# Kernel tuning notes

Measured on AMD Instinct MI355X. Metric: run time of the kernel, lower is better.

Reference implementation:

```python
import jax, jax.numpy as jnp
import numpy as np

N, K, M, D = 50000, 32, 50000, 128  # dst nodes, neighbors, src nodes, hidden_dim


def setup_inputs() -> dict:
    key = jax.random.key(0)
    k1, k2, k3, k4 = jax.random.split(key, 4)
    nei = jax.random.randint(k1, (N, K), 0, M, dtype=jnp.int64)
    h = jax.random.normal(k2, (M, D), dtype=jnp.float32)
    h_refer = jax.random.normal(k3, (N, D), dtype=jnp.float32)
    # xavier_normal_ on (1, 2D) with gain=1.414: std = gain*sqrt(2/(1+2D))
    std = 1.414 * np.sqrt(2.0 / (1 + 2 * D))
    att = jax.random.normal(k4, (1, 2 * D), dtype=jnp.float32) * std
    return {"nei": nei, "h": h, "h_refer": h_refer, "att": att}


def reference(nei, h, h_refer, att):
    # gather neighbor embeddings: [N, K, D]
    nei_emb = h[nei]
    # split att so we never materialize the concatenated [N, K, 2D] tensor:
    # cat([h_refer, nei_emb], -1) @ att.T == h_refer @ att_ref + nei_emb @ att_nei
    att_ref = att[0, :D]   # [D]
    att_nei = att[0, D:]   # [D]
    scores = (h_refer @ att_ref)[:, None] + jnp.einsum("nkd,d->nk", nei_emb, att_nei)  # [N, K]
    scores = jax.nn.leaky_relu(scores, negative_slope=0.01)
    w = jax.nn.softmax(scores, axis=1)  # softmax over neighbors
    # weighted sum over neighbors -> [N, D]
    return jnp.einsum("nk,nkd->nd", w, nei_emb)
```

## Files before the change

kernel.cpp:

```cpp
#include <hip/hip_runtime.h>

typedef unsigned int uint32;
typedef unsigned long long uint64;
typedef unsigned short ushort_t;
typedef _Float16 h2_t __attribute__((ext_vector_type(2)));
typedef float f32x2 __attribute__((ext_vector_type(2)));

#define KNEI 32
#define DIM 128
#define WPB 4

enum { SRC_BF16 = 0, SRC_F16 = 1, SRC_F32 = 2 };

__device__ __forceinline__ float bflo(uint32 u) {
    union { uint32 u; float f; } c; c.u = u << 16; return c.f;
}
__device__ __forceinline__ float bfhi(uint32 u) {
    union { uint32 u; float f; } c; c.u = u & 0xffff0000u; return c.f;
}
__device__ __forceinline__ uint32 pack_bf16_rne(float a, float b) {
    union { float f; uint32 u; } x, y; x.f = a; y.f = b;
    uint32 ua = (x.u + 0x7fffu + ((x.u >> 16) & 1u)) >> 16;
    uint32 ub = (y.u + 0x7fffu + ((y.u >> 16) & 1u)) >> 16;
    return (ua & 0xffffu) | (ub << 16);
}
__device__ __forceinline__ uint32 pack_f16(float a, float b) {
    union { h2_t h; uint32 u; } c;
    c.h.x = (_Float16)a; c.h.y = (_Float16)b;
    return c.u;
}
__device__ __forceinline__ h2_t as_h2(uint32 u) {
    union { uint32 u; h2_t h; } c; c.u = u; return c.h;
}

__device__ __forceinline__ bool probe_bf16(const void* h, int lane) {
    const uint32 hs = ((const uint32*)h)[lane];
    const uint32 e  = (hs >> 7) & 0xFFu;
    const bool  tb  = (e >= 90u) && (e <= 140u);
    return (__ballot(tb) == ~0ull);
}

template<int SRC>
__device__ __forceinline__ void run_row(
    const void* __restrict__ hsv, const void* __restrict__ hrv,
    const void* __restrict__ attv, void* __restrict__ outv,
    const void* __restrict__ neiv, bool i64, int Mrows, int n, int lane)
{
    constexpr bool F32 = (SRC != SRC_BF16);
    const int r4 = lane >> 4;
    const int c  = lane & 15;

    int idxv;
    if (i64) idxv = (int)__builtin_nontemporal_load(
                        (const long long*)neiv + (size_t)n * KNEI + (lane & 31));
    else     idxv = __builtin_nontemporal_load(
                        (const int*)neiv + (size_t)n * KNEI + (lane & 31));
    idxv = min(max(idxv, 0), Mrows - 1);

    int rows[8];
    #pragma unroll
    for (int it = 0; it < 8; ++it)
        rows[it] = __shfl(idxv, it * 4 + r4, 64);

    uint4 ev[8];
    #pragma unroll
    for (int it = 0; it < 8; ++it) {
        if constexpr (SRC == SRC_F32) {
            const float4* sp = (const float4*)hsv + ((size_t)rows[it] << 5) + c * 2;
            const float4 p0 = sp[0], p1 = sp[1];
            ev[it].x = pack_f16(p0.x, p0.y);
            ev[it].y = pack_f16(p0.z, p0.w);
            ev[it].z = pack_f16(p1.x, p1.y);
            ev[it].w = pack_f16(p1.z, p1.w);
        } else {
            ev[it] = *((const uint4*)hsv + ((size_t)rows[it] << 4) + c);
        }
    }

    float base;
    {
        float b0, b1, a0, a1;
        if (F32) {
            const f32x2 hp = __builtin_nontemporal_load(
                (const f32x2*)((const float*)hrv + (size_t)n * DIM) + lane);
            const float2 ap = *((const float2*)attv + lane);
            b0 = hp.x; b1 = hp.y; a0 = ap.x; a1 = ap.y;
        } else {
            const uint32 hu = __builtin_nontemporal_load(
                (const uint32*)((const ushort_t*)hrv + (size_t)n * DIM) + lane);
            const uint32 au = ((const uint32*)attv)[lane];
            b0 = bflo(hu); b1 = bfhi(hu); a0 = bflo(au); a1 = bfhi(au);
        }
        base = b0 * a0 + b1 * a1;
        #pragma unroll
        for (int off = 32; off >= 1; off >>= 1)
            base += __shfl_xor(base, off, 64);
    }

    float an[8];
    if (F32) {
        const float4* ap = (const float4*)((const float*)attv + DIM + c * 8);
        const float4 p0 = ap[0], p1 = ap[1];
        an[0] = p0.x; an[1] = p0.y; an[2] = p0.z; an[3] = p0.w;
        an[4] = p1.x; an[5] = p1.y; an[6] = p1.z; an[7] = p1.w;
    } else {
        const uint4 au = *((const uint4*)((const ushort_t*)attv + DIM) + c);
        an[0] = bflo(au.x); an[1] = bfhi(au.x); an[2] = bflo(au.y); an[3] = bfhi(au.y);
        an[4] = bflo(au.z); an[5] = bfhi(au.z); an[6] = bflo(au.w); an[7] = bfhi(au.w);
    }

    float s[8];
    #pragma unroll
    for (int it = 0; it < 8; ++it) {
        const uint4 e = ev[it];
        if constexpr (SRC == SRC_BF16) {
            s[it] = bflo(e.x) * an[0] + bfhi(e.x) * an[1]
                  + bflo(e.y) * an[2] + bfhi(e.y) * an[3]
                  + bflo(e.z) * an[4] + bfhi(e.z) * an[5]
                  + bflo(e.w) * an[6] + bfhi(e.w) * an[7];
        } else {
            const h2_t e0 = as_h2(e.x), e1 = as_h2(e.y), e2 = as_h2(e.z), e3 = as_h2(e.w);
            const float t0 = fmaf((float)e0.x, an[0],
                             fmaf((float)e0.y, an[1],
                             fmaf((float)e1.x, an[2], (float)e1.y * an[3])));
            const float t1 = fmaf((float)e2.x, an[4],
                             fmaf((float)e2.y, an[5],
                             fmaf((float)e3.x, an[6], (float)e3.y * an[7])));
            s[it] = t0 + t1;
        }
    }
    #pragma unroll
    for (int off = 1; off <= 8; off <<= 1) {
        #pragma unroll
        for (int it = 0; it < 8; ++it)
            s[it] += __shfl_xor(s[it], off, 64);
    }
    #pragma unroll
    for (int it = 0; it < 8; ++it) {
        const float v = base + s[it];
        s[it] = (v > 0.f) ? v : 0.01f * v;
    }

    float m = s[0];
    #pragma unroll
    for (int it = 1; it < 8; ++it) m = fmaxf(m, s[it]);
    m = fmaxf(m, __shfl_xor(m, 16, 64));
    m = fmaxf(m, __shfl_xor(m, 32, 64));

    float w[8];
    float sum = 0.f;
    #pragma unroll
    for (int it = 0; it < 8; ++it) { w[it] = __expf(s[it] - m); sum += w[it]; }
    sum += __shfl_xor(sum, 16, 64);
    sum += __shfl_xor(sum, 32, 64);
    const float inv = 1.0f / sum;

    float acc[8] = {0.f, 0.f, 0.f, 0.f, 0.f, 0.f, 0.f, 0.f};
    #pragma unroll
    for (int it = 0; it < 8; ++it) {
        const float wk = w[it] * inv;
        const uint4 e = ev[it];
        if constexpr (SRC == SRC_BF16) {
            acc[0] = fmaf(wk, bflo(e.x), acc[0]);
            acc[1] = fmaf(wk, bfhi(e.x), acc[1]);
            acc[2] = fmaf(wk, bflo(e.y), acc[2]);
            acc[3] = fmaf(wk, bfhi(e.y), acc[3]);
            acc[4] = fmaf(wk, bflo(e.z), acc[4]);
            acc[5] = fmaf(wk, bfhi(e.z), acc[5]);
            acc[6] = fmaf(wk, bflo(e.w), acc[6]);
            acc[7] = fmaf(wk, bfhi(e.w), acc[7]);
        } else {
            const h2_t e0 = as_h2(e.x), e1 = as_h2(e.y), e2 = as_h2(e.z), e3 = as_h2(e.w);
            acc[0] = fmaf(wk, (float)e0.x, acc[0]);
            acc[1] = fmaf(wk, (float)e0.y, acc[1]);
            acc[2] = fmaf(wk, (float)e1.x, acc[2]);
            acc[3] = fmaf(wk, (float)e1.y, acc[3]);
            acc[4] = fmaf(wk, (float)e2.x, acc[4]);
            acc[5] = fmaf(wk, (float)e2.y, acc[5]);
            acc[6] = fmaf(wk, (float)e3.x, acc[6]);
            acc[7] = fmaf(wk, (float)e3.y, acc[7]);
        }
    }
    #pragma unroll
    for (int d = 0; d < 8; ++d) acc[d] += __shfl_xor(acc[d], 16, 64);
    #pragma unroll
    for (int d = 0; d < 8; ++d) acc[d] += __shfl_xor(acc[d], 32, 64);

    const float q0a = (r4 & 2) ? acc[4] : acc[0];
    const float q0b = (r4 & 2) ? acc[5] : acc[1];
    const float q1a = (r4 & 2) ? acc[6] : acc[2];
    const float q1b = (r4 & 2) ? acc[7] : acc[3];
    const float o0 = (r4 & 1) ? q1a : q0a;
    const float o1 = (r4 & 1) ? q1b : q0b;

    if (F32) {
        f32x2 o; o.x = o0; o.y = o1;
        *((f32x2*)((float*)outv + (size_t)n * DIM) + c * 4 + r4) = o;
    } else {
        ((uint32*)((ushort_t*)outv + (size_t)n * DIM))[c * 4 + r4] = pack_bf16_rne(o0, o1);
    }
}

__global__ __launch_bounds__(256) void gat_kernel(
    const void* __restrict__ nei, const void* __restrict__ h,
    const void* __restrict__ h_refer, const void* __restrict__ att,
    void* __restrict__ out, const void* __restrict__ hf16,
    int N, int Mrows, int use_ws)
{
    const int tid  = threadIdx.x;
    const int lane = tid & 63;
    const int n    = blockIdx.x * WPB + (tid >> 6);

    const bool is_bf16 = probe_bf16(h, lane);
    const uint32 nhi = ((const uint32*)nei)[2 * lane + 1];
    const bool  i64  = (__ballot(nhi == 0u) == ~0ull);

    if (n >= N) return;

    if (is_bf16)     run_row<SRC_BF16>(h,    h_refer, att, out, nei, i64, Mrows, n, lane);
    else if (use_ws) run_row<SRC_F16 >(hf16, h_refer, att, out, nei, i64, Mrows, n, lane);
    else             run_row<SRC_F32 >(h,    h_refer, att, out, nei, i64, Mrows, n, lane);
}

__global__ __launch_bounds__(256) void conv_kernel(
    const void* __restrict__ h, uint4* __restrict__ ws, long long ngroups)
{
    if (probe_bf16(h, threadIdx.x & 63)) return;
    const long long i = (long long)blockIdx.x * 256 + threadIdx.x;
    if (i >= ngroups) return;
    const float4* sp = (const float4*)h + i * 2;
    const float4 p0 = sp[0], p1 = sp[1];
    uint4 o;
    o.x = pack_f16(p0.x, p0.y);
    o.y = pack_f16(p0.z, p0.w);
    o.z = pack_f16(p1.x, p1.y);
    o.w = pack_f16(p1.z, p1.w);
    ws[i] = o;
}

extern "C" void kernel_launch(void* const* d_in, const int* in_sizes, int n_in,
                              void* d_out, int out_size, void* d_ws, size_t ws_size,
                              hipStream_t stream) {
    const int N = out_size / DIM;
    const int M = in_sizes[1] / DIM;

    const size_t need = (size_t)M * DIM * sizeof(ushort_t);
    const int use_ws = (d_ws != nullptr && ws_size >= need) ? 1 : 0;

    if (use_ws) {
        const long long ngroups = (long long)M * (DIM / 8);
        dim3 cg((unsigned)((ngroups + 255) / 256)), cb(256);
        conv_kernel<<<cg, cb, 0, stream>>>(d_in[1], (uint4*)d_ws, ngroups);
    }

    dim3 grid((N + WPB - 1) / WPB), block(64 * WPB);
    gat_kernel<<<grid, block, 0, stream>>>(d_in[0], d_in[1], d_in[2], d_in[3],
                                           d_out, d_ws, N, M, use_ws);
}
```

Measured before the change: 150.5 us.

## Process two destination rows per wavefront to double gathers in flight

Each wavefront now handles two destination nodes. It loads all 64 neighbor indices in one load and issues the gathers for both rows before computing either, which doubles memory-level parallelism per wave. The h_refer dot product for both rows is computed together, and stores and conv loads become nontemporal. In exchange, register pressure rises because 16 uint4 gather buffers are live at once, which may reduce occupancy, and the grid has half as many waves.

```diff
diff --git a/kernel.cpp b/kernel.cpp
--- a/kernel.cpp
+++ b/kernel.cpp
@@ -4,11 +4,14 @@
 typedef unsigned long long uint64;
 typedef unsigned short ushort_t;
 typedef _Float16 h2_t __attribute__((ext_vector_type(2)));
-typedef float f32x2 __attribute__((ext_vector_type(2)));
+typedef float  f32x2 __attribute__((ext_vector_type(2)));
+typedef float  f32x4 __attribute__((ext_vector_type(4)));
+typedef uint32 u32x2 __attribute__((ext_vector_type(2)));
 
 #define KNEI 32
 #define DIM 128
 #define WPB 4
+#define RPW 2
 
 enum { SRC_BF16 = 0, SRC_F16 = 1, SRC_F32 = 2 };
 
@@ -41,73 +44,11 @@
 }
 
 template<int SRC>
-__device__ __forceinline__ void run_row(
-    const void* __restrict__ hsv, const void* __restrict__ hrv,
-    const void* __restrict__ attv, void* __restrict__ outv,
-    const void* __restrict__ neiv, bool i64, int Mrows, int n, int lane)
+__device__ __forceinline__ void process_row(
+    const uint4* ev, const float* an, float base,
+    void* __restrict__ outv, size_t n, int lane, int r4, int c)
 {
     constexpr bool F32 = (SRC != SRC_BF16);
-    const int r4 = lane >> 4;
-    const int c  = lane & 15;
-
-    int idxv;
-    if (i64) idxv = (int)__builtin_nontemporal_load(
-                        (const long long*)neiv + (size_t)n * KNEI + (lane & 31));
-    else     idxv = __builtin_nontemporal_load(
-                        (const int*)neiv + (size_t)n * KNEI + (lane & 31));
-    idxv = min(max(idxv, 0), Mrows - 1);
-
-    int rows[8];
-    #pragma unroll
-    for (int it = 0; it < 8; ++it)
-        rows[it] = __shfl(idxv, it * 4 + r4, 64);
-
-    uint4 ev[8];
-    #pragma unroll
-    for (int it = 0; it < 8; ++it) {
-        if constexpr (SRC == SRC_F32) {
-            const float4* sp = (const float4*)hsv + ((size_t)rows[it] << 5) + c * 2;
-            const float4 p0 = sp[0], p1 = sp[1];
-            ev[it].x = pack_f16(p0.x, p0.y);
-            ev[it].y = pack_f16(p0.z, p0.w);
-            ev[it].z = pack_f16(p1.x, p1.y);
-            ev[it].w = pack_f16(p1.z, p1.w);
-        } else {
-            ev[it] = *((const uint4*)hsv + ((size_t)rows[it] << 4) + c);
-        }
-    }
-
-    float base;
-    {
-        float b0, b1, a0, a1;
-        if (F32) {
-            const f32x2 hp = __builtin_nontemporal_load(
-                (const f32x2*)((const float*)hrv + (size_t)n * DIM) + lane);
-            const float2 ap = *((const float2*)attv + lane);
-            b0 = hp.x; b1 = hp.y; a0 = ap.x; a1 = ap.y;
-        } else {
-            const uint32 hu = __builtin_nontemporal_load(
-                (const uint32*)((const ushort_t*)hrv + (size_t)n * DIM) + lane);
-            const uint32 au = ((const uint32*)attv)[lane];
-            b0 = bflo(hu); b1 = bfhi(hu); a0 = bflo(au); a1 = bfhi(au);
-        }
-        base = b0 * a0 + b1 * a1;
-        #pragma unroll
-        for (int off = 32; off >= 1; off >>= 1)
-            base += __shfl_xor(base, off, 64);
-    }
-
-    float an[8];
-    if (F32) {
-        const float4* ap = (const float4*)((const float*)attv + DIM + c * 8);
-        const float4 p0 = ap[0], p1 = ap[1];
-        an[0] = p0.x; an[1] = p0.y; an[2] = p0.z; an[3] = p0.w;
-        an[4] = p1.x; an[5] = p1.y; an[6] = p1.z; an[7] = p1.w;
-    } else {
-        const uint4 au = *((const uint4*)((const ushort_t*)attv + DIM) + c);
-        an[0] = bflo(au.x); an[1] = bfhi(au.x); an[2] = bflo(au.y); an[3] = bfhi(au.y);
-        an[4] = bflo(au.z); an[5] = bfhi(au.z); an[6] = bflo(au.w); an[7] = bfhi(au.w);
-    }
 
     float s[8];
     #pragma unroll
@@ -195,10 +136,103 @@
 
     if (F32) {
         f32x2 o; o.x = o0; o.y = o1;
-        *((f32x2*)((float*)outv + (size_t)n * DIM) + c * 4 + r4) = o;
+        __builtin_nontemporal_store(o, (f32x2*)((float*)outv + n * DIM) + c * 4 + r4);
     } else {
-        ((uint32*)((ushort_t*)outv + (size_t)n * DIM))[c * 4 + r4] = pack_bf16_rne(o0, o1);
-    }
+        __builtin_nontemporal_store(pack_bf16_rne(o0, o1),
+            (uint32*)((ushort_t*)outv + n * DIM) + c * 4 + r4);
+    }
+}
+
+template<int SRC>
+__device__ __forceinline__ void run_two(
+    const void* __restrict__ hsv, const void* __restrict__ hrv,
+    const void* __restrict__ attv, void* __restrict__ outv,
+    const void* __restrict__ neiv, bool i64, int Mrows,
+    int n0, bool valid2, int lane)
+{
+    constexpr bool F32 = (SRC != SRC_BF16);
+    const int r4 = lane >> 4;
+    const int c  = lane & 15;
+
+    const size_t ebase = (size_t)n0 * KNEI;
+    const int esel = valid2 ? lane : (lane & 31);
+    int idxv;
+    if (i64) idxv = (int)__builtin_nontemporal_load((const long long*)neiv + ebase + esel);
+    else     idxv = __builtin_nontemporal_load((const int*)neiv + ebase + esel);
+    idxv = min(max(idxv, 0), Mrows - 1);
+
+    int rows_a[8], rows_b[8];
+    #pragma unroll
+    for (int it = 0; it < 8; ++it) {
+        rows_a[it] = __shfl(idxv, it * 4 + r4, 64);
+        rows_b[it] = __shfl(idxv, 32 + it * 4 + r4, 64);
+    }
+
+    uint4 eva[8], evb[8];
+    #pragma unroll
+    for (int it = 0; it < 8; ++it) {
+        if constexpr (SRC == SRC_F32) {
+            const float4* sp = (const float4*)hsv + ((size_t)rows_a[it] << 5) + c * 2;
+            const float4 p0 = sp[0], p1 = sp[1];
+            eva[it].x = pack_f16(p0.x, p0.y);
+            eva[it].y = pack_f16(p0.z, p0.w);
+            eva[it].z = pack_f16(p1.x, p1.y);
+            eva[it].w = pack_f16(p1.z, p1.w);
+        } else {
+            eva[it] = *((const uint4*)hsv + ((size_t)rows_a[it] << 4) + c);
+        }
+    }
+    #pragma unroll
+    for (int it = 0; it < 8; ++it) {
+        if constexpr (SRC == SRC_F32) {
+            const float4* sp = (const float4*)hsv + ((size_t)rows_b[it] << 5) + c * 2;
+            const float4 p0 = sp[0], p1 = sp[1];
+            evb[it].x = pack_f16(p0.x, p0.y);
+            evb[it].y = pack_f16(p0.z, p0.w);
+            evb[it].z = pack_f16(p1.x, p1.y);
+            evb[it].w = pack_f16(p1.z, p1.w);
+        } else {
+            evb[it] = *((const uint4*)hsv + ((size_t)rows_b[it] << 4) + c);
+        }
+    }
+
+    const int r2 = lane >> 5;
+    const int l5 = lane & 31;
+    const size_t brow = (size_t)n0 + (valid2 ? r2 : 0);
+    float bsum;
+    if (F32) {
+        const f32x4 hp = __builtin_nontemporal_load(
+            (const f32x4*)((const float*)hrv + brow * DIM) + l5);
+        const f32x4 ap = *((const f32x4*)attv + l5);
+        bsum = hp.x * ap.x + hp.y * ap.y + hp.z * ap.z + hp.w * ap.w;
+    } else {
+        const u32x2 hu = __builtin_nontemporal_load(
+            (const u32x2*)((const ushort_t*)hrv + brow * DIM) + l5);
+        const u32x2 au = *((const u32x2*)attv + l5);
+        bsum = bflo(hu.x) * bflo(au.x) + bfhi(hu.x) * bfhi(au.x)
+             + bflo(hu.y) * bflo(au.y) + bfhi(hu.y) * bfhi(au.y);
+    }
+    #pragma unroll
+    for (int off = 1; off <= 16; off <<= 1)
+        bsum += __shfl_xor(bsum, off, 64);
+    const float baseA = __shfl(bsum, 0, 64);
+    const float baseB = __shfl(bsum, 32, 64);
+
+    float an[8];
+    if (F32) {
+        const float4* ap = (const float4*)((const float*)attv + DIM + c * 8);
+        const float4 p0 = ap[0], p1 = ap[1];
+        an[0] = p0.x; an[1] = p0.y; an[2] = p0.z; an[3] = p0.w;
+        an[4] = p1.x; an[5] = p1.y; an[6] = p1.z; an[7] = p1.w;
+    } else {
+        const uint4 au = *((const uint4*)((const ushort_t*)attv + DIM) + c);
+        an[0] = bflo(au.x); an[1] = bfhi(au.x); an[2] = bflo(au.y); an[3] = bfhi(au.y);
+        an[4] = bflo(au.z); an[5] = bfhi(au.z); an[6] = bflo(au.w); an[7] = bfhi(au.w);
+    }
+
+    process_row<SRC>(eva, an, baseA, outv, (size_t)n0, lane, r4, c);
+    if (valid2)
+        process_row<SRC>(evb, an, baseB, outv, (size_t)n0 + 1, lane, r4, c);
 }
 
 __global__ __launch_bounds__(256) void gat_kernel(
@@ -209,17 +243,18 @@
 {
     const int tid  = threadIdx.x;
     const int lane = tid & 63;
-    const int n    = blockIdx.x * WPB + (tid >> 6);
+    const int n0   = (blockIdx.x * WPB + (tid >> 6)) * RPW;
 
     const bool is_bf16 = probe_bf16(h, lane);
     const uint32 nhi = ((const uint32*)nei)[2 * lane + 1];
     const bool  i64  = (__ballot(nhi == 0u) == ~0ull);
 
-    if (n >= N) return;
-
-    if (is_bf16)     run_row<SRC_BF16>(h,    h_refer, att, out, nei, i64, Mrows, n, lane);
-    else if (use_ws) run_row<SRC_F16 >(hf16, h_refer, att, out, nei, i64, Mrows, n, lane);
-    else             run_row<SRC_F32 >(h,    h_refer, att, out, nei, i64, Mrows, n, lane);
+    if (n0 >= N) return;
+    const bool valid2 = (n0 + 1 < N);
+
+    if (is_bf16)     run_two<SRC_BF16>(h,    h_refer, att, out, nei, i64, Mrows, n0, valid2, lane);
+    else if (use_ws) run_two<SRC_F16 >(hf16, h_refer, att, out, nei, i64, Mrows, n0, valid2, lane);
+    else             run_two<SRC_F32 >(h,    h_refer, att, out, nei, i64, Mrows, n0, valid2, lane);
 }
 
 __global__ __launch_bounds__(256) void conv_kernel(
@@ -228,8 +263,9 @@
     if (probe_bf16(h, threadIdx.x & 63)) return;
     const long long i = (long long)blockIdx.x * 256 + threadIdx.x;
     if (i >= ngroups) return;
-    const float4* sp = (const float4*)h + i * 2;
-    const float4 p0 = sp[0], p1 = sp[1];
+    const f32x4* sp = (const f32x4*)h + i * 2;
+    const f32x4 p0 = __builtin_nontemporal_load(sp);
+    const f32x4 p1 = __builtin_nontemporal_load(sp + 1);
     uint4 o;
     o.x = pack_f16(p0.x, p0.y);
     o.y = pack_f16(p0.z, p0.w);
@@ -253,7 +289,8 @@
         conv_kernel<<<cg, cb, 0, stream>>>(d_in[1], (uint4*)d_ws, ngroups);
     }
 
-    dim3 grid((N + WPB - 1) / WPB), block(64 * WPB);
+    const int rows_per_block = WPB * RPW;
+    dim3 grid((N + rows_per_block - 1) / rows_per_block), block(64 * WPB);
     gat_kernel<<<grid, block, 0, stream>>>(d_in[0], d_in[1], d_in[2], d_in[3],
                                            d_out, d_ws, N, M, use_ws);
 }
```

Result: faster. 147.5 us (median of 2 runs) (-2.0%).

## Process eight rows per wavefront with double-buffered neighbor gathers

Applied to the files above, without the earlier changes.

Each wavefront now handles a chunk of eight destination rows and prefetches the next row's neighbor indices and gathered embeddings while the current row is computed, overlapping gather latency with arithmetic. The h_refer dot products for all eight rows are computed together with wider vector loads and a shorter shuffle reduction. Output stores and the conversion kernel's loads become nontemporal. This raises register pressure from two gather buffers and shrinks the grid eight-fold, which may lower occupancy and latency hiding across waves.

```diff
diff --git a/kernel.cpp b/kernel.cpp
--- a/kernel.cpp
+++ b/kernel.cpp
@@ -4,11 +4,14 @@
 typedef unsigned long long uint64;
 typedef unsigned short ushort_t;
 typedef _Float16 h2_t __attribute__((ext_vector_type(2)));
-typedef float f32x2 __attribute__((ext_vector_type(2)));
+typedef float  f32x2 __attribute__((ext_vector_type(2)));
+typedef float  f32x4 __attribute__((ext_vector_type(4)));
+typedef uint32 u32x4 __attribute__((ext_vector_type(4)));
 
 #define KNEI 32
 #define DIM 128
 #define WPB 4
+#define CH  8
 
 enum { SRC_BF16 = 0, SRC_F16 = 1, SRC_F32 = 2 };
 
@@ -40,29 +43,16 @@
     return (__ballot(tb) == ~0ull);
 }
 
+__device__ __forceinline__ int load_idx(const void* __restrict__ neiv, bool i64,
+                                        size_t n, int lane) {
+    const size_t eb = n * KNEI + (lane & 31);
+    if (i64) return (int)__builtin_nontemporal_load((const long long*)neiv + eb);
+    return __builtin_nontemporal_load((const int*)neiv + eb);
+}
+
 template<int SRC>
-__device__ __forceinline__ void run_row(
-    const void* __restrict__ hsv, const void* __restrict__ hrv,
-    const void* __restrict__ attv, void* __restrict__ outv,
-    const void* __restrict__ neiv, bool i64, int Mrows, int n, int lane)
-{
-    constexpr bool F32 = (SRC != SRC_BF16);
-    const int r4 = lane >> 4;
-    const int c  = lane & 15;
-
-    int idxv;
-    if (i64) idxv = (int)__builtin_nontemporal_load(
-                        (const long long*)neiv + (size_t)n * KNEI + (lane & 31));
-    else     idxv = __builtin_nontemporal_load(
-                        (const int*)neiv + (size_t)n * KNEI + (lane & 31));
-    idxv = min(max(idxv, 0), Mrows - 1);
-
-    int rows[8];
-    #pragma unroll
-    for (int it = 0; it < 8; ++it)
-        rows[it] = __shfl(idxv, it * 4 + r4, 64);
-
-    uint4 ev[8];
+__device__ __forceinline__ void gather_tile(const void* __restrict__ hsv,
+                                            const int* rows, int c, uint4* ev) {
     #pragma unroll
     for (int it = 0; it < 8; ++it) {
         if constexpr (SRC == SRC_F32) {
@@ -76,38 +66,14 @@
             ev[it] = *((const uint4*)hsv + ((size_t)rows[it] << 4) + c);
         }
     }
-
-    float base;
-    {
-        float b0, b1, a0, a1;
-        if (F32) {
-            const f32x2 hp = __builtin_nontemporal_load(
-                (const f32x2*)((const float*)hrv + (size_t)n * DIM) + lane);
-            const float2 ap = *((const float2*)attv + lane);
-            b0 = hp.x; b1 = hp.y; a0 = ap.x; a1 = ap.y;
-        } else {
-            const uint32 hu = __builtin_nontemporal_load(
-                (const uint32*)((const ushort_t*)hrv + (size_t)n * DIM) + lane);
-            const uint32 au = ((const uint32*)attv)[lane];
-            b0 = bflo(hu); b1 = bfhi(hu); a0 = bflo(au); a1 = bfhi(au);
-        }
-        base = b0 * a0 + b1 * a1;
-        #pragma unroll
-        for (int off = 32; off >= 1; off >>= 1)
-            base += __shfl_xor(base, off, 64);
-    }
-
-    float an[8];
-    if (F32) {
-        const float4* ap = (const float4*)((const float*)attv + DIM + c * 8);
-        const float4 p0 = ap[0], p1 = ap[1];
-        an[0] = p0.x; an[1] = p0.y; an[2] = p0.z; an[3] = p0.w;
-        an[4] = p1.x; an[5] = p1.y; an[6] = p1.z; an[7] = p1.w;
-    } else {
-        const uint4 au = *((const uint4*)((const ushort_t*)attv + DIM) + c);
-        an[0] = bflo(au.x); an[1] = bfhi(au.x); an[2] = bflo(au.y); an[3] = bfhi(au.y);
-        an[4] = bflo(au.z); an[5] = bfhi(au.z); an[6] = bflo(au.w); an[7] = bfhi(au.w);
-    }
+}
+
+template<int SRC>
+__device__ __forceinline__ void process_row(
+    const uint4* ev, const float* an, float base,
+    void* __restrict__ outv, size_t n, bool store_ok, int lane, int r4, int c)
+{
+    constexpr bool F32 = (SRC != SRC_BF16);
 
     float s[8];
     #pragma unroll
@@ -193,11 +159,104 @@
     const float o0 = (r4 & 1) ? q1a : q0a;
     const float o1 = (r4 & 1) ? q1b : q0b;
 
+    if (store_ok) {
+        if (F32) {
+            f32x2 o; o.x = o0; o.y = o1;
+            __builtin_nontemporal_store(o, (f32x2*)((float*)outv + n * DIM) + c * 4 + r4);
+        } else {
+            __builtin_nontemporal_store(pack_bf16_rne(o0, o1),
+                (uint32*)((ushort_t*)outv + n * DIM) + c * 4 + r4);
+        }
+    }
+}
+
+template<int SRC>
+__device__ __forceinline__ void run_chunk(
+    const void* __restrict__ hsv, const void* __restrict__ hrv,
+    const void* __restrict__ attv, void* __restrict__ outv,
+    const void* __restrict__ neiv, bool i64, int Mrows,
+    size_t n0, int N, int lane)
+{
+    constexpr bool F32 = (SRC != SRC_BF16);
+    const int r4 = lane >> 4;
+    const int c  = lane & 15;
+    const size_t nlast = (size_t)(N - 1);
+
+    int idxA = load_idx(neiv, i64, (n0 < nlast) ? n0 : nlast, lane);
+
+    const int g = lane >> 3, j = lane & 7;
+    const size_t bn = (n0 + g < nlast) ? (n0 + g) : nlast;
+    float bsum = 0.f;
     if (F32) {
-        f32x2 o; o.x = o0; o.y = o1;
-        *((f32x2*)((float*)outv + (size_t)n * DIM) + c * 4 + r4) = o;
+        const f32x4* hp = (const f32x4*)((const float*)hrv + bn * DIM) + j * 4;
+        const f32x4* ap = (const f32x4*)attv + j * 4;
+        #pragma unroll
+        for (int k2 = 0; k2 < 4; ++k2) {
+            const f32x4 hv = __builtin_nontemporal_load(hp + k2);
+            const f32x4 av = ap[k2];
+            bsum += hv.x * av.x + hv.y * av.y + hv.z * av.z + hv.w * av.w;
+        }
     } else {
-        ((uint32*)((ushort_t*)outv + (size_t)n * DIM))[c * 4 + r4] = pack_bf16_rne(o0, o1);
+        const u32x4* hp = (const u32x4*)((const ushort_t*)hrv + bn * DIM) + j * 2;
+        const u32x4* ap = (const u32x4*)attv + j * 2;
+        #pragma unroll
+        for (int k2 = 0; k2 < 2; ++k2) {
+            const u32x4 hv = __builtin_nontemporal_load(hp + k2);
+            const u32x4 av = ap[k2];
+            bsum += bflo(hv.x) * bflo(av.x) + bfhi(hv.x) * bfhi(av.x)
+                  + bflo(hv.y) * bflo(av.y) + bfhi(hv.y) * bfhi(av.y)
+                  + bflo(hv.z) * bflo(av.z) + bfhi(hv.z) * bfhi(av.z)
+                  + bflo(hv.w) * bflo(av.w) + bfhi(hv.w) * bfhi(av.w);
+        }
+    }
+    #pragma unroll
+    for (int off = 1; off <= 4; off <<= 1)
+        bsum += __shfl_xor(bsum, off, 64);
+    float base[CH];
+    #pragma unroll
+    for (int g2 = 0; g2 < CH; ++g2)
+        base[g2] = __shfl(bsum, g2 << 3, 64);
+
+    float an[8];
+    if (F32) {
+        const float4* ap = (const float4*)((const float*)attv + DIM + c * 8);
+        const float4 p0 = ap[0], p1 = ap[1];
+        an[0] = p0.x; an[1] = p0.y; an[2] = p0.z; an[3] = p0.w;
+        an[4] = p1.x; an[5] = p1.y; an[6] = p1.z; an[7] = p1.w;
+    } else {
+        const uint4 au = *((const uint4*)((const ushort_t*)attv + DIM) + c);
+        an[0] = bflo(au.x); an[1] = bfhi(au.x); an[2] = bflo(au.y); an[3] = bfhi(au.y);
+        an[4] = bflo(au.z); an[5] = bfhi(au.z); an[6] = bflo(au.w); an[7] = bfhi(au.w);
+    }
+
+    uint4 ev0[8], ev1[8];
+    {
+        const int ic = min(max(idxA, 0), Mrows - 1);
+        int rows[8];
+        #pragma unroll
+        for (int it = 0; it < 8; ++it) rows[it] = __shfl(ic, it * 4 + r4, 64);
+        gather_tile<SRC>(hsv, rows, c, ev0);
+    }
+    int idxB = load_idx(neiv, i64, (n0 + 1 < nlast) ? (n0 + 1) : nlast, lane);
+
+    #pragma unroll
+    for (int i = 0; i < CH; ++i) {
+        uint4* evc = (i & 1) ? ev1 : ev0;
+        uint4* evn = (i & 1) ? ev0 : ev1;
+        if (i + 1 < CH) {
+            const int idxn = (i & 1) ? idxA : idxB;
+            const int ic = min(max(idxn, 0), Mrows - 1);
+            int rows[8];
+            #pragma unroll
+            for (int it = 0; it < 8; ++it) rows[it] = __shfl(ic, it * 4 + r4, 64);
+            gather_tile<SRC>(hsv, rows, c, evn);
+        }
+        if (i + 2 < CH) {
+            const size_t nn = (n0 + i + 2 < nlast) ? (n0 + i + 2) : nlast;
+            const int nx = load_idx(neiv, i64, nn, lane);
+            if (i & 1) idxB = nx; else idxA = nx;
+        }
+        process_row<SRC>(evc, an, base[i], outv, n0 + i, (n0 + i) <= nlast, lane, r4, c);
     }
 }
 
@@ -209,17 +268,17 @@
 {
     const int tid  = threadIdx.x;
     const int lane = tid & 63;
-    const int n    = blockIdx.x * WPB + (tid >> 6);
+    const size_t n0 = ((size_t)blockIdx.x * WPB + (tid >> 6)) * CH;
 
     const bool is_bf16 = probe_bf16(h, lane);
     const uint32 nhi = ((const uint32*)nei)[2 * lane + 1];
     const bool  i64  = (__ballot(nhi == 0u) == ~0ull);
 
-    if (n >= N) return;
-
-    if (is_bf16)     run_row<SRC_BF16>(h,    h_refer, att, out, nei, i64, Mrows, n, lane);
-    else if (use_ws) run_row<SRC_F16 >(hf16, h_refer, att, out, nei, i64, Mrows, n, lane);
-    else             run_row<SRC_F32 >(h,    h_refer, att, out, nei, i64, Mrows, n, lane);
+    if (n0 >= (size_t)N) return;
+
+    if (is_bf16)     run_chunk<SRC_BF16>(h,    h_refer, att, out, nei, i64, Mrows, n0, N, lane);
+    else if (use_ws) run_chunk<SRC_F16 >(hf16, h_refer, att, out, nei, i64, Mrows, n0, N, lane);
+    else             run_chunk<SRC_F32 >(h,    h_refer, att, out, nei, i64, Mrows, n0, N, lane);
 }
 
 __global__ __launch_bounds__(256) void conv_kernel(
@@ -228,8 +287,9 @@
     if (probe_bf16(h, threadIdx.x & 63)) return;
     const long long i = (long long)blockIdx.x * 256 + threadIdx.x;
     if (i >= ngroups) return;
-    const float4* sp = (const float4*)h + i * 2;
-    const float4 p0 = sp[0], p1 = sp[1];
+    const f32x4* sp = (const f32x4*)h + i * 2;
+    const f32x4 p0 = __builtin_nontemporal_load(sp);
+    const f32x4 p1 = __builtin_nontemporal_load(sp + 1);
     uint4 o;
     o.x = pack_f16(p0.x, p0.y);
     o.y = pack_f16(p0.z, p0.w);
@@ -253,7 +313,8 @@
         conv_kernel<<<cg, cb, 0, stream>>>(d_in[1], (uint4*)d_ws, ngroups);
     }
 
-    dim3 grid((N + WPB - 1) / WPB), block(64 * WPB);
+    const int rows_per_block = WPB * CH;
+    dim3 grid((N + rows_per_block - 1) / rows_per_block), block(64 * WPB);
     gat_kernel<<<grid, block, 0, stream>>>(d_in[0], d_in[1], d_in[2], d_in[3],
                                            d_out, d_ws, N, M, use_ws);
 }
```

Result: slower. 165.9 us (+10.2%).
